# Kernel tuning notes

Measured on AMD Instinct MI355X. Metric: run time of the kernel, lower is better.

Reference implementation:

```python
import jax, jax.numpy as jnp
import numpy as np

B, N, F, L, H, C = 128, 512, 128, 64, 128, 10

def setup_inputs() -> dict:
    key = jax.random.key(0)
    ks = jax.random.split(key, 20)
    s = 0.1
    return {
        "g": jax.random.uniform(ks[0], (B, N, N), dtype=jnp.float32) + 1e-3,
        "h": jax.random.normal(ks[1], (B, N, F), dtype=jnp.float32),
        "labels": jax.random.randint(ks[2], (B,), 0, C),
        "eps": jax.random.normal(ks[3], (B, N, 1), dtype=jnp.float32),
        "W_s": jax.random.normal(ks[4], (F, L), dtype=jnp.float32) * s,
        "b_s": jnp.zeros((L,), jnp.float32),
        "W_mu": jax.random.normal(ks[5], (L, 1), dtype=jnp.float32) * s,
        "b_mu": jnp.zeros((1,), jnp.float32),
        "W_lv": jax.random.normal(ks[6], (L, 1), dtype=jnp.float32) * s,
        "b_lv": jnp.zeros((1,), jnp.float32),
        "W_dec": jax.random.normal(ks[7], (1, L), dtype=jnp.float32) * s,
        "b_dec": jnp.zeros((L,), jnp.float32),
        "W1": jax.random.normal(ks[8], (L, H), dtype=jnp.float32) * s,
        "b1": jnp.zeros((H,), jnp.float32),
        "W2": jax.random.normal(ks[9], (H, C), dtype=jnp.float32) * s,
        "b2": jnp.zeros((C,), jnp.float32),
        "beta": jnp.array([50.0], jnp.float32),
    }

def _gcn(gn, x, W, b):
    # GCN layer: propagate then project then ELU activation (dropout = 0)
    return jax.nn.elu(jnp.einsum('bnm,bmf->bnf', gn, x) @ W + b)

def reference(g, h, labels, eps, W_s, b_s, W_mu, b_mu, W_lv, b_lv, W_dec, b_dec, W1, b1, W2, b2, beta):
    # norm_g: degrees = sum over dim 1; broadcast division normalizes COLUMNS
    # (torch g/degrees with degrees of shape [N] divides g[:, j] by degrees[j])
    deg = jnp.sum(g, axis=1)                      # [B, N]
    gn = g / deg[:, None, :]                      # column-normalized adjacency
    h1 = _gcn(gn, h, W_s, b_s)                    # [B, N, L]
    mu = _gcn(gn, h1, W_mu, b_mu)                 # [B, N, 1]
    lv = _gcn(gn, h1, W_lv, b_lv)                 # [B, N, 1]
    z = mu + eps * jnp.exp(0.5 * lv)              # reparameterize (training)
    v = jax.nn.sigmoid(beta[0] * z)               # [B, N, 1]
    d = _gcn(gn, v, W_dec, b_dec)                 # [B, N, L]
    hp = jnp.einsum('bnl,bn->bl', h1, v[..., 0])  # h.T @ v pooling -> [B, L]
    logits = jax.nn.log_softmax(jax.nn.elu(hp @ W1 + b1) @ W2 + b2, axis=1)
    nll = -jnp.mean(logits[jnp.arange(B), labels])
    mus = mu.reshape(-1, 1)
    lvs = lv.reshape(-1, 1)
    M = mus.shape[0]
    kl = (-0.5 / M) * jnp.mean(jnp.sum(1.0 + 2.0 * lvs - mus**2 - jnp.exp(lvs)**2, axis=1))
    mse = jnp.mean((h1 - d) ** 2)
    loss = nll + kl + mse
    acc = jnp.mean((jnp.argmax(logits, axis=1) == labels).astype(jnp.float32))
    return (loss, acc)
```

## Files before the change

### kernel.cpp

```cpp
#include <hip/hip_runtime.h>

#define B_  128
#define N_  512
#define F_  128
#define L_  64
#define H_  128
#define C_  10

typedef short  bf8_t  __attribute__((ext_vector_type(8)));
typedef float  f32x4  __attribute__((ext_vector_type(4)));
typedef unsigned short us8 __attribute__((ext_vector_type(8)));
typedef unsigned short us4 __attribute__((ext_vector_type(4)));

static __device__ __forceinline__ unsigned short f2bf(float x) {
    union { float f; unsigned u; } c; c.f = x;
    unsigned r = (c.u + 0x7fffu + ((c.u >> 16) & 1u)) >> 16;
    return (unsigned short)r;
}
static __device__ __forceinline__ float bf2f(unsigned short s) {
    union { unsigned u; float f; } c; c.u = ((unsigned)s) << 16;
    return c.f;
}
static __device__ __forceinline__ float elu(float x) { return x > 0.f ? x : expm1f(x); }

#define OFF_DEGP   0
#define OFF_DEG    2097152
#define OFF_HPP    2162688
#define OFF_KLP    2293760
#define OFF_MSEP   2294784
#define OFF_TMU    2296832
#define OFF_TLV    2362368
#define OFF_V      2427904
#define OFF_W      2493440
#define OFF_LP     2558976
#define OFF_COR    2559104
#define OFF_H1Q    2559232
#define OFF_GBF    4656384
#define OFF_UBFT   21433600
#define OFF_WSTBF  23530752

__global__ __launch_bounds__(256) void k1_deg(const float* __restrict__ g,
                                              const float* __restrict__ Ws,
                                              float* __restrict__ deg_part,
                                              unsigned short* __restrict__ gbf,
                                              unsigned short* __restrict__ WsTbf) {
    const int c = blockIdx.x, b = blockIdx.y;
    if (c == 0 && b == 0) {
        for (int i = threadIdx.x; i < F_ * L_; i += 256) {
            int l = i >> 7, f = i & 127;
            WsTbf[i] = f2bf(Ws[f * L_ + l]);
        }
    }
    const int half = threadIdx.x >> 7, lane = threadIdx.x & 127;
    const int j  = lane * 4;
    const int i0 = c * 32 + half * 16;
    const float*    gp = g   + ((size_t)b * N_ + i0) * N_ + j;
    unsigned short* gq = gbf + ((size_t)b * N_ + i0) * N_ + j;
    float4 acc = make_float4(0.f, 0.f, 0.f, 0.f);
    #pragma unroll 8
    for (int r = 0; r < 16; ++r) {
        float4 v = *reinterpret_cast<const float4*>(gp + (size_t)r * N_);
        acc.x += v.x; acc.y += v.y; acc.z += v.z; acc.w += v.w;
        us4 q; q[0] = f2bf(v.x); q[1] = f2bf(v.y); q[2] = f2bf(v.z); q[3] = f2bf(v.w);
        *reinterpret_cast<us4*>(gq + (size_t)r * N_) = q;
    }
    *reinterpret_cast<float4*>(deg_part + (size_t)(b * 32 + c * 2 + half) * N_ + j) = acc;
}

__global__ __launch_bounds__(256) void k2_u(const float* __restrict__ h,
                                            const unsigned short* __restrict__ WsTbf,
                                            const float* __restrict__ deg_part,
                                            float* __restrict__ deg,
                                            unsigned short* __restrict__ ubfT) {
    __shared__ float tile[64 * 65];
    __shared__ float sdeg[64];
    const int b    = blockIdx.y;
    const int m0   = blockIdx.x * 64;
    const int tid  = threadIdx.x;
    const int wave = tid >> 6, lane = tid & 63;
    const int ml = lane & 15, q = lane >> 4;
    const int row0 = wave * 16;

    if (tid < 64) {
        int j = m0 + tid;
        float s = 0.f;
        #pragma unroll
        for (int k = 0; k < 32; ++k) s += deg_part[(size_t)(b * 32 + k) * N_ + j];
        sdeg[tid] = s;
        deg[b * N_ + j] = s;
    }

    const float* A = h + (size_t)(b * N_ + m0 + row0 + ml) * F_ + q * 8;
    const unsigned short* Bb = WsTbf + ml * F_ + q * 8;

    f32x4 acc[4] = {};
    #pragma unroll
    for (int kk = 0; kk < F_; kk += 32) {
        float4 a0 = *reinterpret_cast<const float4*>(A + kk);
        float4 a1 = *reinterpret_cast<const float4*>(A + kk + 4);
        union { unsigned short s[8]; bf8_t v; } av;
        av.s[0] = f2bf(a0.x); av.s[1] = f2bf(a0.y); av.s[2] = f2bf(a0.z); av.s[3] = f2bf(a0.w);
        av.s[4] = f2bf(a1.x); av.s[5] = f2bf(a1.y); av.s[6] = f2bf(a1.z); av.s[7] = f2bf(a1.w);
        #pragma unroll
        for (int i = 0; i < 4; ++i) {
            bf8_t bv = *reinterpret_cast<const bf8_t*>(Bb + i * 16 * F_ + kk);
            acc[i] = __builtin_amdgcn_mfma_f32_16x16x32_bf16(av.v, bv, acc[i], 0, 0, 0);
        }
    }
    __syncthreads();
    #pragma unroll
    for (int i = 0; i < 4; ++i) {
        int col = i * 16 + ml;
        #pragma unroll
        for (int r = 0; r < 4; ++r) {
            int rl = row0 + 4 * q + r;
            tile[rl * 65 + col] = acc[i][r] / sdeg[rl];
        }
    }
    __syncthreads();
    for (int jj = 0; jj < 16; ++jj) {
        int ll = wave + jj * 4;
        ubfT[(size_t)(b * L_ + ll) * N_ + m0 + lane] = f2bf(tile[lane * 65 + ll]);
    }
}

__global__ __launch_bounds__(256) void k3_h1(const unsigned short* __restrict__ gbf,
                                             const unsigned short* __restrict__ ubfT,
                                             const float* __restrict__ b_s,
                                             const float* __restrict__ Wmu,
                                             const float* __restrict__ Wlv,
                                             const float* __restrict__ deg,
                                             unsigned short* __restrict__ h1q,
                                             float* __restrict__ tmu, float* __restrict__ tlv) {
    const int b    = blockIdx.y;
    const int tid  = threadIdx.x;
    const int wave = tid >> 6, lane = tid & 63;
    const int row0 = blockIdx.x * 64 + wave * 16;
    const int ml = lane & 15, q = lane >> 4;

    const unsigned short* A  = gbf  + (size_t)(b * N_ + row0 + ml) * N_ + q * 8;
    const unsigned short* B0 = ubfT + (size_t)(b * L_ + ml) * N_ + q * 8;

    f32x4 acc[4] = {};
    #pragma unroll 4
    for (int k = 0; k < N_; k += 32) {
        bf8_t a = *reinterpret_cast<const bf8_t*>(A + k);
        #pragma unroll
        for (int i = 0; i < 4; ++i) {
            bf8_t bb = *reinterpret_cast<const bf8_t*>(B0 + (size_t)i * 16 * N_ + k);
            acc[i] = __builtin_amdgcn_mfma_f32_16x16x32_bf16(a, bb, acc[i], 0, 0, 0);
        }
    }
    float bsv[4], wm[4], wl[4];
    #pragma unroll
    for (int i = 0; i < 4; ++i) {
        int col = i * 16 + ml;
        bsv[i] = b_s[col]; wm[i] = Wmu[col]; wl[i] = Wlv[col];
    }
    #pragma unroll
    for (int r = 0; r < 4; ++r) {
        int row = row0 + 4 * q + r;
        float pm = 0.f, pl = 0.f;
        #pragma unroll
        for (int i = 0; i < 4; ++i) {
            float hv = elu(acc[i][r] + bsv[i]);
            h1q[(size_t)(b * N_ + row) * L_ + i * 16 + ml] = f2bf(hv);
            pm = fmaf(hv, wm[i], pm);
            pl = fmaf(hv, wl[i], pl);
        }
        #pragma unroll
        for (int o = 1; o < 16; o <<= 1) { pm += __shfl_xor(pm, o); pl += __shfl_xor(pl, o); }
        if (ml == 0) {
            float idg = 1.f / deg[b * N_ + row];
            tmu[b * N_ + row] = pm * idg;
            tlv[b * N_ + row] = pl * idg;
        }
    }
}

__global__ __launch_bounds__(256) void k5_v(const unsigned short* __restrict__ gbf,
                                            const float* __restrict__ tmu, const float* __restrict__ tlv,
                                            const float* __restrict__ eps, const float* __restrict__ deg,
                                            const float* __restrict__ bmu, const float* __restrict__ blv,
                                            const float* __restrict__ beta,
                                            float* __restrict__ v, float* __restrict__ w,
                                            float* __restrict__ kl_part) {
    __shared__ float kls[4];
    const int b = blockIdx.y;
    const int wave = threadIdx.x >> 6, lane = threadIdx.x & 63;
    const int n0 = (blockIdx.x * 4 + wave) * 16;

    const float* tmr = tmu + b * N_ + lane * 8;
    const float* tlr = tlv + b * N_ + lane * 8;
    float tm[8], tl[8];
    *reinterpret_cast<float4*>(tm)     = *reinterpret_cast<const float4*>(tmr);
    *reinterpret_cast<float4*>(tm + 4) = *reinterpret_cast<const float4*>(tmr + 4);
    *reinterpret_cast<float4*>(tl)     = *reinterpret_cast<const float4*>(tlr);
    *reinterpret_cast<float4*>(tl + 4) = *reinterpret_cast<const float4*>(tlr + 4);

    const unsigned short* gbase = gbf + (size_t)(b * N_ + n0) * N_ + lane * 8;
    float myamu = 0.f, myalv = 0.f;
    #pragma unroll 4
    for (int r = 0; r < 16; ++r) {
        us8 gv = *reinterpret_cast<const us8*>(gbase + (size_t)r * N_);
        float amu = 0.f, alv = 0.f;
        #pragma unroll
        for (int j = 0; j < 8; ++j) {
            float gf = bf2f(gv[j]);
            amu = fmaf(gf, tm[j], amu);
            alv = fmaf(gf, tl[j], alv);
        }
        #pragma unroll
        for (int o = 32; o; o >>= 1) { amu += __shfl_xor(amu, o); alv += __shfl_xor(alv, o); }
        if (lane == r) { myamu = amu; myalv = alv; }
    }
    float klv = 0.f;
    if (lane < 16) {
        int n = n0 + lane;
        float mu = elu(myamu + bmu[0]);
        float lv = elu(myalv + blv[0]);
        float z  = mu + eps[b * N_ + n] * expf(0.5f * lv);
        float vv = 1.f / (1.f + expf(-beta[0] * z));
        v[b * N_ + n] = vv;
        w[b * N_ + n] = vv / deg[b * N_ + n];
        float e = expf(lv);
        klv = 1.f + 2.f * lv - mu * mu - e * e;
    }
    #pragma unroll
    for (int o = 32; o; o >>= 1) klv += __shfl_xor(klv, o);
    if (lane == 0) kls[wave] = klv;
    __syncthreads();
    if (threadIdx.x == 0)
        kl_part[blockIdx.y * 8 + blockIdx.x] = kls[0] + kls[1] + kls[2] + kls[3];
}

__global__ __launch_bounds__(256) void k6_dec(const unsigned short* __restrict__ gbf,
                                              const float* __restrict__ w, const float* __restrict__ v,
                                              const unsigned short* __restrict__ h1q,
                                              const float* __restrict__ Wdec, const float* __restrict__ bdec,
                                              float* __restrict__ hp_part, float* __restrict__ mse_part) {
    __shared__ float hps[4 * 64];
    __shared__ float mses[4];
    const int b = blockIdx.y;
    const int n0 = blockIdx.x * 32;
    const int tid = threadIdx.x, wave = tid >> 6, lane = tid & 63;
    const float wd = Wdec[lane], bd = bdec[lane];

    const float* wrow = w + b * N_ + lane * 8;
    float wr[8];
    *reinterpret_cast<float4*>(wr)     = *reinterpret_cast<const float4*>(wrow);
    *reinterpret_cast<float4*>(wr + 4) = *reinterpret_cast<const float4*>(wrow + 4);

    const unsigned short* gbase = gbf + (size_t)(b * N_ + n0 + wave * 8) * N_ + lane * 8;
    float hpl = 0.f, msep = 0.f;
    #pragma unroll 4
    for (int t = 0; t < 8; ++t) {
        int n = n0 + wave * 8 + t;
        us8 gv = *reinterpret_cast<const us8*>(gbase + (size_t)t * N_);
        float p = 0.f;
        #pragma unroll
        for (int j = 0; j < 8; ++j) p = fmaf(bf2f(gv[j]), wr[j], p);
        #pragma unroll
        for (int o = 32; o; o >>= 1) p += __shfl_xor(p, o);
        float dv = elu(p * wd + bd);
        float h1v = bf2f(h1q[(size_t)(b * N_ + n) * L_ + lane]);
        float diff = h1v - dv;
        msep = fmaf(diff, diff, msep);
        hpl  = fmaf(h1v, v[b * N_ + n], hpl);
    }
    hps[wave * 64 + lane] = hpl;
    #pragma unroll
    for (int o = 32; o; o >>= 1) msep += __shfl_xor(msep, o);
    if (lane == 0) mses[wave] = msep;
    __syncthreads();
    if (tid < 64) {
        float s = hps[tid] + hps[64 + tid] + hps[128 + tid] + hps[192 + tid];
        hp_part[(size_t)blockIdx.x * (B_ * 64) + b * 64 + tid] = s;
    }
    if (tid == 0)
        mse_part[blockIdx.y * 16 + blockIdx.x] = mses[0] + mses[1] + mses[2] + mses[3];
}

__global__ __launch_bounds__(128) void k7a_head(const float* __restrict__ hp_part,
                                                const float* __restrict__ W1, const float* __restrict__ b1,
                                                const float* __restrict__ W2, const float* __restrict__ b2,
                                                const int* __restrict__ labels,
                                                float* __restrict__ lp, float* __restrict__ cor) {
    __shared__ float hps[64];
    __shared__ float acts[128];
    __shared__ float lgs[10];
    const int b = blockIdx.x, tid = threadIdx.x;
    if (tid < 64) {
        float s = 0.f;
        #pragma unroll
        for (int x = 0; x < 16; ++x) s += hp_part[(size_t)x * (B_ * 64) + b * 64 + tid];
        hps[tid] = s;
    }
    __syncthreads();
    float s0 = 0, s1 = 0, s2 = 0, s3 = 0;
    for (int l = 0; l < 64; l += 4) {
        s0 += hps[l]     * W1[(l)     * H_ + tid];
        s1 += hps[l + 1] * W1[(l + 1) * H_ + tid];
        s2 += hps[l + 2] * W1[(l + 2) * H_ + tid];
        s3 += hps[l + 3] * W1[(l + 3) * H_ + tid];
    }
    acts[tid] = elu((s0 + s1) + (s2 + s3) + b1[tid]);
    __syncthreads();
    if (tid < C_) {
        float lg = b2[tid];
        for (int hh = 0; hh < H_; ++hh) lg += acts[hh] * W2[hh * C_ + tid];
        lgs[tid] = lg;
    }
    __syncthreads();
    if (tid == 0) {
        float mx = lgs[0]; int am = 0;
        for (int c = 1; c < C_; ++c) if (lgs[c] > mx) { mx = lgs[c]; am = c; }
        float se = 0.f;
        for (int c = 0; c < C_; ++c) se += expf(lgs[c] - mx);
        int lbl = labels[b];
        lp[b]  = lgs[lbl] - mx - logf(se);
        cor[b] = (am == lbl) ? 1.f : 0.f;
    }
}

__global__ __launch_bounds__(128) void k7b_final(const float* __restrict__ lp, const float* __restrict__ cor,
                                                 const float* __restrict__ kl_part, const float* __restrict__ mse_part,
                                                 float* __restrict__ out) {
    __shared__ float r1[128], r2[128], r3[128], r4[128];
    int tid = threadIdx.x;
    r1[tid] = lp[tid]; r2[tid] = cor[tid];
    float k = 0.f, m = 0.f;
    #pragma unroll
    for (int i = 0; i < 8; ++i)  k += kl_part[tid + i * 128];
    #pragma unroll
    for (int i = 0; i < 16; ++i) m += mse_part[tid + i * 128];
    r3[tid] = k; r4[tid] = m;
    __syncthreads();
    for (int o = 64; o; o >>= 1) {
        if (tid < o) { r1[tid] += r1[tid + o]; r2[tid] += r2[tid + o];
                       r3[tid] += r3[tid + o]; r4[tid] += r4[tid + o]; }
        __syncthreads();
    }
    if (tid == 0) {
        float nll = -r1[0] / (float)B_;
        float kl  = r3[0] * (-0.5f / (65536.f * 65536.f));
        float mse = r4[0] / (float)(B_ * N_ * L_);
        out[0] = nll + kl + mse;
        out[1] = r2[0] / (float)B_;
    }
}

extern "C" void kernel_launch(void* const* d_in, const int* in_sizes, int n_in,
                              void* d_out, int out_size, void* d_ws, size_t ws_size,
                              hipStream_t stream) {
    const float* g     = (const float*)d_in[0];
    const float* h     = (const float*)d_in[1];
    const int*   labels= (const int*)  d_in[2];
    const float* eps   = (const float*)d_in[3];
    const float* W_s   = (const float*)d_in[4];
    const float* b_s   = (const float*)d_in[5];
    const float* W_mu  = (const float*)d_in[6];
    const float* b_mu  = (const float*)d_in[7];
    const float* W_lv  = (const float*)d_in[8];
    const float* b_lv  = (const float*)d_in[9];
    const float* W_dec = (const float*)d_in[10];
    const float* b_dec = (const float*)d_in[11];
    const float* W1    = (const float*)d_in[12];
    const float* b1    = (const float*)d_in[13];
    const float* W2    = (const float*)d_in[14];
    const float* b2    = (const float*)d_in[15];
    const float* beta  = (const float*)d_in[16];

    float* ws = (float*)d_ws;
    float* deg_part = ws + OFF_DEGP;
    float* deg      = ws + OFF_DEG;
    float* hp_part  = ws + OFF_HPP;
    float* kl_part  = ws + OFF_KLP;
    float* mse_part = ws + OFF_MSEP;
    float* tmu      = ws + OFF_TMU;
    float* tlv      = ws + OFF_TLV;
    float* vv       = ws + OFF_V;
    float* wv       = ws + OFF_W;
    float* lp       = ws + OFF_LP;
    float* cor      = ws + OFF_COR;
    unsigned short* h1q   = (unsigned short*)(ws + OFF_H1Q);
    unsigned short* gbf   = (unsigned short*)(ws + OFF_GBF);
    unsigned short* ubfT  = (unsigned short*)(ws + OFF_UBFT);
    unsigned short* WsTbf = (unsigned short*)(ws + OFF_WSTBF);

    k1_deg  <<<dim3(16, B_), 256, 0, stream>>>(g, W_s, deg_part, gbf, WsTbf);
    k2_u    <<<dim3(8, B_), 256, 0, stream>>>(h, WsTbf, deg_part, deg, ubfT);
    k3_h1   <<<dim3(8, B_), 256, 0, stream>>>(gbf, ubfT, b_s, W_mu, W_lv, deg, h1q, tmu, tlv);
    k5_v    <<<dim3(8, B_), 256, 0, stream>>>(gbf, tmu, tlv, eps, deg, b_mu, b_lv, beta, vv, wv, kl_part);
    k6_dec  <<<dim3(16, B_), 256, 0, stream>>>(gbf, wv, vv, h1q, W_dec, b_dec, hp_part, mse_part);
    k7a_head<<<B_, 128, 0, stream>>>(hp_part, W1, b1, W2, b2, labels, lp, cor);
    k7b_final<<<1, 128, 0, stream>>>(lp, cor, kl_part, mse_part, (float*)d_out);
}
```

Before: 336.1 us.

## Use MFMA for matrix-vector propagations in k5/k6 and widen k1 loads

The two matrix-vector products over the normalized adjacency (the mu/logvar propagation in k5 and the decoder propagation in k6) now run as bf16 MFMA instructions instead of scalar FMAs followed by cross-lane shuffle reductions. The mu and logvar vectors are interleaved into the B operand. The intermediate vectors tmu, tlv and w are stored as bf16 to feed the MFMAs. k6 now handles 16 rows per wave, so its grid and partial-sum counts drop from 16 to 8. k1 uses 8-wide loads and stores per lane with half as many blocks. This removes shuffle-reduction overhead, at the cost of extra bf16 rounding on the propagated vectors and some lane-broadcast shuffles.

```diff
diff --git a/kernel.cpp b/kernel.cpp
--- a/kernel.cpp
+++ b/kernel.cpp
@@ -10,7 +10,6 @@
 typedef short  bf8_t  __attribute__((ext_vector_type(8)));
 typedef float  f32x4  __attribute__((ext_vector_type(4)));
 typedef unsigned short us8 __attribute__((ext_vector_type(8)));
-typedef unsigned short us4 __attribute__((ext_vector_type(4)));
 
 static __device__ __forceinline__ unsigned short f2bf(float x) {
     union { float f; unsigned u; } c; c.f = x;
@@ -26,45 +25,51 @@
 #define OFF_DEGP   0
 #define OFF_DEG    2097152
 #define OFF_HPP    2162688
-#define OFF_KLP    2293760
-#define OFF_MSEP   2294784
-#define OFF_TMU    2296832
-#define OFF_TLV    2362368
-#define OFF_V      2427904
-#define OFF_W      2493440
-#define OFF_LP     2558976
-#define OFF_COR    2559104
-#define OFF_H1Q    2559232
-#define OFF_GBF    4656384
-#define OFF_UBFT   21433600
-#define OFF_WSTBF  23530752
+#define OFF_KLP    2228224
+#define OFF_MSEP   2229248
+#define OFF_V      2230272
+#define OFF_LP     2295808
+#define OFF_COR    2295936
+#define OFF_TMUBF  2296064
+#define OFF_TLVBF  2328832
+#define OFF_WVBF   2361600
+#define OFF_H1Q    2394368
+#define OFF_GBF    4491520
+#define OFF_UBFT   21268736
+#define OFF_WSTBF  23365888
 
 __global__ __launch_bounds__(256) void k1_deg(const float* __restrict__ g,
                                               const float* __restrict__ Ws,
                                               float* __restrict__ deg_part,
                                               unsigned short* __restrict__ gbf,
                                               unsigned short* __restrict__ WsTbf) {
-    const int c = blockIdx.x, b = blockIdx.y;
-    if (c == 0 && b == 0) {
+    const int c8 = blockIdx.x, b = blockIdx.y;
+    if (c8 == 0 && b == 0) {
         for (int i = threadIdx.x; i < F_ * L_; i += 256) {
             int l = i >> 7, f = i & 127;
             WsTbf[i] = f2bf(Ws[f * L_ + l]);
         }
     }
-    const int half = threadIdx.x >> 7, lane = threadIdx.x & 127;
-    const int j  = lane * 4;
-    const int i0 = c * 32 + half * 16;
-    const float*    gp = g   + ((size_t)b * N_ + i0) * N_ + j;
-    unsigned short* gq = gbf + ((size_t)b * N_ + i0) * N_ + j;
-    float4 acc = make_float4(0.f, 0.f, 0.f, 0.f);
-    #pragma unroll 8
+    const int w = threadIdx.x >> 6, lane = threadIdx.x & 63;
+    const int r0 = c8 * 64 + w * 16;
+    const float*    gp = g   + ((size_t)b * N_ + r0) * N_ + lane * 8;
+    unsigned short* gq = gbf + ((size_t)b * N_ + r0) * N_ + lane * 8;
+    float cs[8] = {};
+    #pragma unroll 4
     for (int r = 0; r < 16; ++r) {
-        float4 v = *reinterpret_cast<const float4*>(gp + (size_t)r * N_);
-        acc.x += v.x; acc.y += v.y; acc.z += v.z; acc.w += v.w;
-        us4 q; q[0] = f2bf(v.x); q[1] = f2bf(v.y); q[2] = f2bf(v.z); q[3] = f2bf(v.w);
-        *reinterpret_cast<us4*>(gq + (size_t)r * N_) = q;
-    }
-    *reinterpret_cast<float4*>(deg_part + (size_t)(b * 32 + c * 2 + half) * N_ + j) = acc;
+        float4 v0 = *reinterpret_cast<const float4*>(gp + (size_t)r * N_);
+        float4 v1 = *reinterpret_cast<const float4*>(gp + (size_t)r * N_ + 4);
+        cs[0] += v0.x; cs[1] += v0.y; cs[2] += v0.z; cs[3] += v0.w;
+        cs[4] += v1.x; cs[5] += v1.y; cs[6] += v1.z; cs[7] += v1.w;
+        us8 qv;
+        qv[0] = f2bf(v0.x); qv[1] = f2bf(v0.y); qv[2] = f2bf(v0.z); qv[3] = f2bf(v0.w);
+        qv[4] = f2bf(v1.x); qv[5] = f2bf(v1.y); qv[6] = f2bf(v1.z); qv[7] = f2bf(v1.w);
+        *reinterpret_cast<us8*>(gq + (size_t)r * N_) = qv;
+    }
+    const int s = c8 * 4 + w;
+    float* dp = deg_part + ((size_t)(b * 32 + s)) * N_ + lane * 8;
+    *reinterpret_cast<float4*>(dp)     = make_float4(cs[0], cs[1], cs[2], cs[3]);
+    *reinterpret_cast<float4*>(dp + 4) = make_float4(cs[4], cs[5], cs[6], cs[7]);
 }
 
 __global__ __launch_bounds__(256) void k2_u(const float* __restrict__ h,
@@ -131,7 +136,8 @@
                                              const float* __restrict__ Wlv,
                                              const float* __restrict__ deg,
                                              unsigned short* __restrict__ h1q,
-                                             float* __restrict__ tmu, float* __restrict__ tlv) {
+                                             unsigned short* __restrict__ tmubf,
+                                             unsigned short* __restrict__ tlvbf) {
     const int b    = blockIdx.y;
     const int tid  = threadIdx.x;
     const int wave = tid >> 6, lane = tid & 63;
@@ -172,101 +178,101 @@
         for (int o = 1; o < 16; o <<= 1) { pm += __shfl_xor(pm, o); pl += __shfl_xor(pl, o); }
         if (ml == 0) {
             float idg = 1.f / deg[b * N_ + row];
-            tmu[b * N_ + row] = pm * idg;
-            tlv[b * N_ + row] = pl * idg;
+            tmubf[b * N_ + row] = f2bf(pm * idg);
+            tlvbf[b * N_ + row] = f2bf(pl * idg);
         }
     }
 }
 
 __global__ __launch_bounds__(256) void k5_v(const unsigned short* __restrict__ gbf,
-                                            const float* __restrict__ tmu, const float* __restrict__ tlv,
+                                            const unsigned short* __restrict__ tmubf,
+                                            const unsigned short* __restrict__ tlvbf,
                                             const float* __restrict__ eps, const float* __restrict__ deg,
                                             const float* __restrict__ bmu, const float* __restrict__ blv,
                                             const float* __restrict__ beta,
-                                            float* __restrict__ v, float* __restrict__ w,
+                                            float* __restrict__ vv, unsigned short* __restrict__ wvbf,
                                             float* __restrict__ kl_part) {
     __shared__ float kls[4];
     const int b = blockIdx.y;
     const int wave = threadIdx.x >> 6, lane = threadIdx.x & 63;
+    const int ml = lane & 15, q = lane >> 4;
     const int n0 = (blockIdx.x * 4 + wave) * 16;
 
-    const float* tmr = tmu + b * N_ + lane * 8;
-    const float* tlr = tlv + b * N_ + lane * 8;
-    float tm[8], tl[8];
-    *reinterpret_cast<float4*>(tm)     = *reinterpret_cast<const float4*>(tmr);
-    *reinterpret_cast<float4*>(tm + 4) = *reinterpret_cast<const float4*>(tmr + 4);
-    *reinterpret_cast<float4*>(tl)     = *reinterpret_cast<const float4*>(tlr);
-    *reinterpret_cast<float4*>(tl + 4) = *reinterpret_cast<const float4*>(tlr + 4);
-
-    const unsigned short* gbase = gbf + (size_t)(b * N_ + n0) * N_ + lane * 8;
-    float myamu = 0.f, myalv = 0.f;
-    #pragma unroll 4
-    for (int r = 0; r < 16; ++r) {
-        us8 gv = *reinterpret_cast<const us8*>(gbase + (size_t)r * N_);
-        float amu = 0.f, alv = 0.f;
-        #pragma unroll
-        for (int j = 0; j < 8; ++j) {
-            float gf = bf2f(gv[j]);
-            amu = fmaf(gf, tm[j], amu);
-            alv = fmaf(gf, tl[j], alv);
-        }
-        #pragma unroll
-        for (int o = 32; o; o >>= 1) { amu += __shfl_xor(amu, o); alv += __shfl_xor(alv, o); }
-        if (lane == r) { myamu = amu; myalv = alv; }
-    }
+    const unsigned short* A  = gbf + (size_t)(b * N_ + n0 + ml) * N_ + q * 8;
+    const unsigned short* Bp = ((ml & 1) ? tlvbf : tmubf) + (size_t)b * N_ + q * 8;
+
+    f32x4 acc = {};
+    #pragma unroll
+    for (int k = 0; k < N_; k += 32) {
+        bf8_t a  = *reinterpret_cast<const bf8_t*>(A + k);
+        bf8_t bb = *reinterpret_cast<const bf8_t*>(Bp + k);
+        acc = __builtin_amdgcn_mfma_f32_16x16x32_bf16(a, bb, acc, 0, 0, 0);
+    }
+    float alv4[4];
+    #pragma unroll
+    for (int r = 0; r < 4; ++r) alv4[r] = __shfl_xor(acc[r], 1);
+
     float klv = 0.f;
-    if (lane < 16) {
-        int n = n0 + lane;
-        float mu = elu(myamu + bmu[0]);
-        float lv = elu(myalv + blv[0]);
-        float z  = mu + eps[b * N_ + n] * expf(0.5f * lv);
-        float vv = 1.f / (1.f + expf(-beta[0] * z));
-        v[b * N_ + n] = vv;
-        w[b * N_ + n] = vv / deg[b * N_ + n];
-        float e = expf(lv);
-        klv = 1.f + 2.f * lv - mu * mu - e * e;
-    }
-    #pragma unroll
-    for (int o = 32; o; o >>= 1) klv += __shfl_xor(klv, o);
+    if (ml == 0) {
+        const float bmu0 = bmu[0], blv0 = blv[0], beta0 = beta[0];
+        #pragma unroll
+        for (int r = 0; r < 4; ++r) {
+            int n = n0 + 4 * q + r;
+            float mu = elu(acc[r] + bmu0);
+            float lv = elu(alv4[r] + blv0);
+            float z  = mu + eps[b * N_ + n] * expf(0.5f * lv);
+            float vs = 1.f / (1.f + expf(-beta0 * z));
+            vv[b * N_ + n]   = vs;
+            wvbf[b * N_ + n] = f2bf(vs / deg[b * N_ + n]);
+            float e = expf(lv);
+            klv += 1.f + 2.f * lv - mu * mu - e * e;
+        }
+    }
+    klv += __shfl_xor(klv, 16);
+    klv += __shfl_xor(klv, 32);
     if (lane == 0) kls[wave] = klv;
     __syncthreads();
     if (threadIdx.x == 0)
-        kl_part[blockIdx.y * 8 + blockIdx.x] = kls[0] + kls[1] + kls[2] + kls[3];
+        kl_part[b * 8 + blockIdx.x] = kls[0] + kls[1] + kls[2] + kls[3];
 }
 
 __global__ __launch_bounds__(256) void k6_dec(const unsigned short* __restrict__ gbf,
-                                              const float* __restrict__ w, const float* __restrict__ v,
+                                              const unsigned short* __restrict__ wvbf,
+                                              const float* __restrict__ vv,
                                               const unsigned short* __restrict__ h1q,
                                               const float* __restrict__ Wdec, const float* __restrict__ bdec,
                                               float* __restrict__ hp_part, float* __restrict__ mse_part) {
     __shared__ float hps[4 * 64];
     __shared__ float mses[4];
     const int b = blockIdx.y;
-    const int n0 = blockIdx.x * 32;
     const int tid = threadIdx.x, wave = tid >> 6, lane = tid & 63;
+    const int ml = lane & 15, q = lane >> 4;
+    const int n0 = (blockIdx.x * 4 + wave) * 16;
+
+    const unsigned short* A  = gbf  + (size_t)(b * N_ + n0 + ml) * N_ + q * 8;
+    const unsigned short* Bp = wvbf + (size_t)b * N_ + q * 8;
+
+    f32x4 acc = {};
+    #pragma unroll
+    for (int k = 0; k < N_; k += 32) {
+        bf8_t a  = *reinterpret_cast<const bf8_t*>(A + k);
+        bf8_t bb = *reinterpret_cast<const bf8_t*>(Bp + k);
+        acc = __builtin_amdgcn_mfma_f32_16x16x32_bf16(a, bb, acc, 0, 0, 0);
+    }
+    float pbc[16];
+    #pragma unroll
+    for (int t = 0; t < 16; ++t) pbc[t] = __shfl(acc[t & 3], (t >> 2) << 4);
+
     const float wd = Wdec[lane], bd = bdec[lane];
-
-    const float* wrow = w + b * N_ + lane * 8;
-    float wr[8];
-    *reinterpret_cast<float4*>(wr)     = *reinterpret_cast<const float4*>(wrow);
-    *reinterpret_cast<float4*>(wr + 4) = *reinterpret_cast<const float4*>(wrow + 4);
-
-    const unsigned short* gbase = gbf + (size_t)(b * N_ + n0 + wave * 8) * N_ + lane * 8;
     float hpl = 0.f, msep = 0.f;
     #pragma unroll 4
-    for (int t = 0; t < 8; ++t) {
-        int n = n0 + wave * 8 + t;
-        us8 gv = *reinterpret_cast<const us8*>(gbase + (size_t)t * N_);
-        float p = 0.f;
-        #pragma unroll
-        for (int j = 0; j < 8; ++j) p = fmaf(bf2f(gv[j]), wr[j], p);
-        #pragma unroll
-        for (int o = 32; o; o >>= 1) p += __shfl_xor(p, o);
-        float dv = elu(p * wd + bd);
+    for (int t = 0; t < 16; ++t) {
+        int n = n0 + t;
+        float dv  = elu(pbc[t] * wd + bd);
         float h1v = bf2f(h1q[(size_t)(b * N_ + n) * L_ + lane]);
         float diff = h1v - dv;
         msep = fmaf(diff, diff, msep);
-        hpl  = fmaf(h1v, v[b * N_ + n], hpl);
+        hpl  = fmaf(h1v, vv[b * N_ + n], hpl);
     }
     hps[wave * 64 + lane] = hpl;
     #pragma unroll
@@ -278,7 +284,7 @@
         hp_part[(size_t)blockIdx.x * (B_ * 64) + b * 64 + tid] = s;
     }
     if (tid == 0)
-        mse_part[blockIdx.y * 16 + blockIdx.x] = mses[0] + mses[1] + mses[2] + mses[3];
+        mse_part[b * 8 + blockIdx.x] = mses[0] + mses[1] + mses[2] + mses[3];
 }
 
 __global__ __launch_bounds__(128) void k7a_head(const float* __restrict__ hp_part,
@@ -293,7 +299,7 @@
     if (tid < 64) {
         float s = 0.f;
         #pragma unroll
-        for (int x = 0; x < 16; ++x) s += hp_part[(size_t)x * (B_ * 64) + b * 64 + tid];
+        for (int x = 0; x < 8; ++x) s += hp_part[(size_t)x * (B_ * 64) + b * 64 + tid];
         hps[tid] = s;
     }
     __syncthreads();
@@ -333,7 +339,7 @@
     #pragma unroll
     for (int i = 0; i < 8; ++i)  k += kl_part[tid + i * 128];
     #pragma unroll
-    for (int i = 0; i < 16; ++i) m += mse_part[tid + i * 128];
+    for (int i = 0; i < 8; ++i)  m += mse_part[tid + i * 128];
     r3[tid] = k; r4[tid] = m;
     __syncthreads();
     for (int o = 64; o; o >>= 1) {
@@ -377,22 +383,22 @@
     float* hp_part  = ws + OFF_HPP;
     float* kl_part  = ws + OFF_KLP;
     float* mse_part = ws + OFF_MSEP;
-    float* tmu      = ws + OFF_TMU;
-    float* tlv      = ws + OFF_TLV;
     float* vv       = ws + OFF_V;
-    float* wv       = ws + OFF_W;
     float* lp       = ws + OFF_LP;
     float* cor      = ws + OFF_COR;
+    unsigned short* tmubf = (unsigned short*)(ws + OFF_TMUBF);
+    unsigned short* tlvbf = (unsigned short*)(ws + OFF_TLVBF);
+    unsigned short* wvbf  = (unsigned short*)(ws + OFF_WVBF);
     unsigned short* h1q   = (unsigned short*)(ws + OFF_H1Q);
     unsigned short* gbf   = (unsigned short*)(ws + OFF_GBF);
     unsigned short* ubfT  = (unsigned short*)(ws + OFF_UBFT);
     unsigned short* WsTbf = (unsigned short*)(ws + OFF_WSTBF);
 
-    k1_deg  <<<dim3(16, B_), 256, 0, stream>>>(g, W_s, deg_part, gbf, WsTbf);
+    k1_deg  <<<dim3(8, B_), 256, 0, stream>>>(g, W_s, deg_part, gbf, WsTbf);
     k2_u    <<<dim3(8, B_), 256, 0, stream>>>(h, WsTbf, deg_part, deg, ubfT);
-    k3_h1   <<<dim3(8, B_), 256, 0, stream>>>(gbf, ubfT, b_s, W_mu, W_lv, deg, h1q, tmu, tlv);
-    k5_v    <<<dim3(8, B_), 256, 0, stream>>>(gbf, tmu, tlv, eps, deg, b_mu, b_lv, beta, vv, wv, kl_part);
-    k6_dec  <<<dim3(16, B_), 256, 0, stream>>>(gbf, wv, vv, h1q, W_dec, b_dec, hp_part, mse_part);
+    k3_h1   <<<dim3(8, B_), 256, 0, stream>>>(gbf, ubfT, b_s, W_mu, W_lv, deg, h1q, tmubf, tlvbf);
+    k5_v    <<<dim3(8, B_), 256, 0, stream>>>(gbf, tmubf, tlvbf, eps, deg, b_mu, b_lv, beta, vv, wvbf, kl_part);
+    k6_dec  <<<dim3(8, B_), 256, 0, stream>>>(gbf, wvbf, vv, h1q, W_dec, b_dec, hp_part, mse_part);
     k7a_head<<<B_, 128, 0, stream>>>(hp_part, W1, b1, W2, b2, labels, lp, cor);
     k7b_final<<<1, 128, 0, stream>>>(lp, cor, kl_part, mse_part, (float*)d_out);
 }
```

Result: no change. 342.0 us (+1.8%).
